# Kernel optimization log

Hardware: AMD Instinct MI355X
Metric: run time of the kernel (lower is better)

## Reference

```python
import jax, jax.numpy as jnp
import numpy as np

N_NODES = 100000
N_EDGES = 3200000
NUM_TYPES = 8
TYPE_DIM = 16
IN_DIM = 5
HID = 64
HEADS = 2
OUT = 64
LN_EPS = 1e-5
NEG_SLOPE = 0.2


def segment_softmax(logits, seg, num_segments):
    # logits: [E, H], seg: [E] destination ids
    m = jax.ops.segment_max(logits, seg, num_segments=num_segments)
    m = jnp.where(jnp.isfinite(m), m, 0.0)
    e = jnp.exp(logits - m[seg])
    s = jax.ops.segment_sum(e, seg, num_segments=num_segments)
    return e / (s[seg] + 1e-16)


def gat_conv(x, W, a_src, a_dst, b, src, dst, n_nodes, heads, ch):
    # x: [N, F_in], W: [F_in, heads*ch], a_src/a_dst: [heads, ch], b: [heads*ch]
    h = (x @ W).reshape(n_nodes, heads, ch)            # [N, H, C]
    al_s = jnp.einsum('nhc,hc->nh', h, a_src)          # [N, H]
    al_d = jnp.einsum('nhc,hc->nh', h, a_dst)          # [N, H]
    e = jax.nn.leaky_relu(al_s[src] + al_d[dst], NEG_SLOPE)  # [E, H]
    alpha = segment_softmax(e, dst, n_nodes)           # [E, H]
    msg = alpha[:, :, None] * h[src]                   # [E, H, C]
    out = jax.ops.segment_sum(msg, dst, num_segments=n_nodes)  # [N, H, C]
    return out.reshape(n_nodes, heads * ch) + b


def setup_inputs() -> dict:
    key = jax.random.key(0)
    ks = jax.random.split(key, 16)
    in1 = IN_DIM + TYPE_DIM  # 21
    inp = {
        'x': jax.random.normal(ks[0], (N_NODES, IN_DIM), dtype=jnp.float32),
        'edge_index': jax.random.randint(ks[1], (2, N_EDGES), 0, N_NODES, dtype=jnp.int32),
        'type_ids': jax.random.randint(ks[2], (N_NODES,), 0, NUM_TYPES, dtype=jnp.int32),
        'type_emb': jax.random.normal(ks[3], (NUM_TYPES, TYPE_DIM), dtype=jnp.float32) * 0.3,
        'W1': jax.random.normal(ks[4], (in1, HID), dtype=jnp.float32) * (1.0 / np.sqrt(in1)),
        'a_src1': jax.random.normal(ks[5], (HEADS, HID // HEADS), dtype=jnp.float32) * 0.1,
        'a_dst1': jax.random.normal(ks[6], (HEADS, HID // HEADS), dtype=jnp.float32) * 0.1,
        'b1': jnp.zeros((HID,), dtype=jnp.float32),
        'W2': jax.random.normal(ks[7], (HID, OUT), dtype=jnp.float32) * (1.0 / np.sqrt(HID)),
        'a_src2': jax.random.normal(ks[8], (1, OUT), dtype=jnp.float32) * 0.1,
        'a_dst2': jax.random.normal(ks[9], (1, OUT), dtype=jnp.float32) * 0.1,
        'b2': jnp.zeros((OUT,), dtype=jnp.float32),
        'gamma': jnp.ones((OUT,), dtype=jnp.float32),
        'beta': jnp.zeros((OUT,), dtype=jnp.float32),
    }
    return inp


def reference(x, type_emb, W1, a_src1, a_dst1, b1, W2, a_src2, a_dst2, b2, gamma, beta, edge_index, type_ids):
    n = x.shape[0]
    # type embedding concat
    xin = jnp.concatenate([x, type_emb[type_ids]], axis=1)  # [N, 21]
    # add self loops (PyG GATConv default)
    loops = jnp.arange(n, dtype=edge_index.dtype)
    src = jnp.concatenate([edge_index[0], loops])
    dst = jnp.concatenate([edge_index[1], loops])
    h = gat_conv(xin, W1, a_src1, a_dst1, b1, src, dst, n, HEADS, HID // HEADS)
    h = jax.nn.relu(h)  # dropout = identity at inference
    h = gat_conv(h, W2, a_src2, a_dst2, b2, src, dst, n, 1, OUT)
    # LayerNorm
    mu = jnp.mean(h, axis=-1, keepdims=True)
    var = jnp.var(h, axis=-1, keepdims=True)
    return (h - mu) / jnp.sqrt(var + LN_EPS) * gamma + beta
```

## Files before the change

### kernel.cpp

```cpp
#include <hip/hip_runtime.h>
#include <hip/hip_fp16.h>

#define NEG_SLOPE 0.2f
#define BKT_SHIFT 8
#define BKT_NODES 256
#define BKT_CAP 10240
#define SRC_SHIFT 18
#define SRC_MASK 0x3FFFF
#define CHUNK 4096
#define NBMAX 512

typedef _Float16 half8 __attribute__((ext_vector_type(8)));
typedef float float4v __attribute__((ext_vector_type(4)));

__global__ void k_node1(const float* __restrict__ x, const int* __restrict__ type_ids,
                        const float* __restrict__ type_emb, const float* __restrict__ W1,
                        const float* __restrict__ a_src1, const float* __restrict__ a_dst1,
                        __half2* __restrict__ h1h, float* __restrict__ als1, float* __restrict__ ald1,
                        int N)
{
    int node = blockIdx.x * 4 + (threadIdx.x >> 6);
    int j = threadIdx.x & 63;
    if (node >= N) return;

    float xin[21];
#pragma unroll
    for (int k = 0; k < 5; k++) xin[k] = x[node * 5 + k];
    int t = type_ids[node];
#pragma unroll
    for (int k = 0; k < 16; k++) xin[5 + k] = type_emb[t * 16 + k];

    float h = 0.f;
#pragma unroll
    for (int k = 0; k < 21; k++) h += xin[k] * W1[k * 64 + j];

    float hn = __shfl_xor(h, 1);
    if ((j & 1) == 0)
        h1h[node * 32 + (j >> 1)] = __floats2half2_rn(h, hn);

    int head = j >> 5, lane = j & 31;
    float ps = h * a_src1[head * 32 + lane];
    float pd = h * a_dst1[head * 32 + lane];
#pragma unroll
    for (int m = 16; m >= 1; m >>= 1) { ps += __shfl_xor(ps, m); pd += __shfl_xor(pd, m); }
    if (lane == 0) { als1[node * 2 + head] = ps; ald1[node * 2 + head] = pd; }
}

__global__ void k_bucketA(const int* __restrict__ ei, unsigned int* __restrict__ pk,
                          int* __restrict__ bcnt, int E, int NBKT)
{
    __shared__ unsigned int stage[CHUNK];
    __shared__ unsigned short stageB[CHUNK];
    __shared__ int cnt[NBMAX];
    __shared__ int excl[NBMAX];
    __shared__ int curp[NBMAX];
    __shared__ int gbase[NBMAX];

    int t = threadIdx.x;
    int e0 = blockIdx.x * CHUNK;
    bool vec4 = ((E & 3) == 0);

    for (int i = t; i < NBMAX; i += 256) cnt[i] = 0;
    __syncthreads();

    int4 s4[4], d4[4];
    bool val[4];

    if (vec4) {
#pragma unroll
        for (int it = 0; it < 4; it++) {
            int e = e0 + it * 1024 + t * 4;
            val[it] = (e < E);
            if (val[it]) {
                s4[it] = *(const int4*)(ei + e);
                d4[it] = *(const int4*)(ei + (size_t)E + e);
                atomicAdd(&cnt[d4[it].x >> BKT_SHIFT], 1);
                atomicAdd(&cnt[d4[it].y >> BKT_SHIFT], 1);
                atomicAdd(&cnt[d4[it].z >> BKT_SHIFT], 1);
                atomicAdd(&cnt[d4[it].w >> BKT_SHIFT], 1);
            }
        }
    } else {
        for (int i = t; i < CHUNK; i += 256) {
            int e = e0 + i;
            if (e >= E) break;
            atomicAdd(&cnt[ei[E + e] >> BKT_SHIFT], 1);
        }
    }
    __syncthreads();
    for (int i = t; i < NBMAX; i += 256) curp[i] = cnt[i];
    __syncthreads();
    for (int off = 1; off < NBMAX; off <<= 1) {
        int v0 = (t >= off) ? cnt[t - off] : 0;
        int v1 = (t + 256 >= off) ? cnt[t + 256 - off] : 0;
        __syncthreads();
        cnt[t] += v0; cnt[t + 256] += v1;
        __syncthreads();
    }
    for (int i = t; i < NBMAX; i += 256) {
        int o = curp[i];
        int ex = cnt[i] - o;
        excl[i] = ex;
        curp[i] = ex;
    }
    __syncthreads();
    for (int b = t; b < NBKT; b += 256) {
        int c = cnt[b] - excl[b];
        gbase[b] = (c > 0) ? atomicAdd(&bcnt[b], c) : 0;
    }
    __syncthreads();
    if (vec4) {
#pragma unroll
        for (int it = 0; it < 4; it++) {
            if (!val[it]) continue;
            int ss[4] = {s4[it].x, s4[it].y, s4[it].z, s4[it].w};
            int dd[4] = {d4[it].x, d4[it].y, d4[it].z, d4[it].w};
#pragma unroll
            for (int k = 0; k < 4; k++) {
                int b = dd[k] >> BKT_SHIFT;
                int p = atomicAdd(&curp[b], 1);
                stage[p] = (unsigned)ss[k] | ((unsigned)(dd[k] & (BKT_NODES - 1)) << SRC_SHIFT);
                stageB[p] = (unsigned short)b;
            }
        }
    } else {
        for (int i = t; i < CHUNK; i += 256) {
            int e = e0 + i;
            if (e >= E) break;
            int s = ei[e], d = ei[E + e];
            int b = d >> BKT_SHIFT;
            int p = atomicAdd(&curp[b], 1);
            stage[p] = (unsigned)s | ((unsigned)(d & (BKT_NODES - 1)) << SRC_SHIFT);
            stageB[p] = (unsigned short)b;
        }
    }
    __syncthreads();
    int total = E - e0; if (total > CHUNK) total = CHUNK;
    for (int i = t; i < total; i += 256) {
        int b = stageB[i];
        int idx = gbase[b] + (i - excl[b]);
        if (idx < BKT_CAP) pk[(size_t)b * BKT_CAP + idx] = stage[i];
    }
}

__global__ void k_build(const unsigned int* __restrict__ pk, const int* __restrict__ bcnt,
                        int* __restrict__ rs, int* __restrict__ cur,
                        int* __restrict__ ssrc, int N)
{
    __shared__ unsigned int vals[BKT_CAP];
    __shared__ int cnt[BKT_NODES];
    __shared__ int cursor[BKT_NODES];
    __shared__ int orig[BKT_NODES];
    __shared__ int red[256];
    int b = blockIdx.x;
    int t = threadIdx.x;
    int nb = min(bcnt[b], BKT_CAP);

    int part = 0;
    for (int i = t; i < b; i += 256) part += min(bcnt[i], BKT_CAP);
    red[t] = part;
    cnt[t] = 0;
    __syncthreads();
    for (int off = 128; off; off >>= 1) {
        if (t < off) red[t] += red[t + off];
        __syncthreads();
    }
    int bs = red[0];

    const unsigned int* mypk = pk + (size_t)b * BKT_CAP;
    int nb4 = nb & ~3;
    for (int e = t * 4; e < nb4; e += 1024) {
        uint4 v = *(const uint4*)(mypk + e);
        *(uint4*)(vals + e) = v;
        atomicAdd(&cnt[v.x >> SRC_SHIFT], 1);
        atomicAdd(&cnt[v.y >> SRC_SHIFT], 1);
        atomicAdd(&cnt[v.z >> SRC_SHIFT], 1);
        atomicAdd(&cnt[v.w >> SRC_SHIFT], 1);
    }
    for (int e = nb4 + t; e < nb; e += 256) {
        unsigned int v = mypk[e];
        vals[e] = v;
        atomicAdd(&cnt[v >> SRC_SHIFT], 1);
    }
    __syncthreads();
    orig[t] = cnt[t];
    __syncthreads();
    for (int off = 1; off < BKT_NODES; off <<= 1) {
        int v = (t >= off) ? cnt[t - off] : 0;
        __syncthreads();
        cnt[t] += v;
        __syncthreads();
    }
    {
        int c = orig[t];
        int ex = cnt[t] - c;
        cursor[t] = ex;
        int node = (b << BKT_SHIFT) + t;
        if (node < N) { rs[node] = bs + ex; cur[node] = bs + ex + c; }
    }
    __syncthreads();
    for (int e = t; e < nb; e += 256) {
        unsigned int w = vals[e];
        int p = atomicAdd(&cursor[w >> SRC_SHIFT], 1);
        ssrc[bs + p] = (int)(w & SRC_MASK);
    }
}

__global__ void k_gather1(const int* __restrict__ rs, const int* __restrict__ cur,
                          const int* __restrict__ ssrc, const float4* __restrict__ h4,
                          const float* __restrict__ als1, const float* __restrict__ ald1,
                          const float* __restrict__ b1, float4* __restrict__ h2h4, int N)
{
    int node = blockIdx.x * 4 + (threadIdx.x >> 6);
    if (node >= N) return;
    int l = threadIdx.x & 63;
    int eg = l >> 3;
    int ch = l & 7;
    int head = ch >> 2;
    float ad = ald1[node * 2 + head];

    int beg = rs[node], end = cur[node];
    int cnt = end - beg;
    __half2 acc2[4];
    acc2[0] = acc2[1] = acc2[2] = acc2[3] = __float2half2_rn(0.f);
    float wsum = 0.f;

    int s0n = (eg < cnt) ? ssrc[beg + eg] : node;
    int s1n = (8 + eg < cnt) ? ssrc[beg + 8 + eg] : node;

    for (int base = 0; base < cnt; base += 16) {
        int s0 = s0n, s1 = s1n;
        bool v0 = (base + eg) < cnt, v1 = (base + 8 + eg) < cnt;
        int n0 = base + 16 + eg, n1 = base + 24 + eg;
        s0n = (n0 < cnt) ? ssrc[beg + n0] : node;
        s1n = (n1 < cnt) ? ssrc[beg + n1] : node;

        float al0 = als1[s0 * 2 + head];
        float al1 = als1[s1 * 2 + head];
        float4 r0 = h4[(size_t)s0 * 8 + ch];
        float4 r1 = h4[(size_t)s1 * 8 + ch];
        float lg0 = al0 + ad; lg0 = (lg0 >= 0.f) ? lg0 : NEG_SLOPE * lg0;
        float lg1 = al1 + ad; lg1 = (lg1 >= 0.f) ? lg1 : NEG_SLOPE * lg1;
        float w0 = v0 ? __expf(lg0) : 0.f;
        float w1 = v1 ? __expf(lg1) : 0.f;
        __half2 wh0 = __float2half2_rn(w0);
        __half2 wh1 = __float2half2_rn(w1);
        const __half2* p0 = (const __half2*)&r0;
        const __half2* p1 = (const __half2*)&r1;
#pragma unroll
        for (int q = 0; q < 4; q++) {
            acc2[q] = __hfma2(p0[q], wh0, acc2[q]);
            acc2[q] = __hfma2(p1[q], wh1, acc2[q]);
        }
        wsum += w0 + w1;
    }
    float acc[8];
#pragma unroll
    for (int q = 0; q < 4; q++) {
        float2 f = __half22float2(acc2[q]);
        acc[2*q] = f.x; acc[2*q+1] = f.y;
    }
#pragma unroll
    for (int m = 8; m <= 32; m <<= 1) {
        wsum += __shfl_xor(wsum, m);
#pragma unroll
        for (int q = 0; q < 8; q++) acc[q] += __shfl_xor(acc[q], m);
    }
    {
        float lg = als1[node * 2 + head] + ad;
        lg = (lg >= 0.f) ? lg : NEG_SLOPE * lg;
        float w = __expf(lg);
        float4 r = h4[(size_t)node * 8 + ch];
        const __half2* p = (const __half2*)&r;
#pragma unroll
        for (int q = 0; q < 4; q++) {
            float2 f = __half22float2(p[q]);
            acc[2*q] += w * f.x; acc[2*q+1] += w * f.y;
        }
        wsum += w;
    }
    float inv = 1.f / (wsum + 1e-16f);
    if (eg == 0) {
        union { float4 f4; __half2 h2[4]; } u;
#pragma unroll
        for (int q = 0; q < 4; q++) {
            float v0 = fmaxf(acc[2*q]   * inv + b1[ch * 8 + 2*q],     0.f);
            float v1 = fmaxf(acc[2*q+1] * inv + b1[ch * 8 + 2*q + 1], 0.f);
            u.h2[q] = __floats2half2_rn(v0, v1);
        }
        h2h4[(size_t)node * 8 + ch] = u.f4;
    }
}

__global__ __launch_bounds__(256) void k_node2m(
        const _Float16* __restrict__ h2h, const float* __restrict__ W2,
        const float* __restrict__ a_src2, const float* __restrict__ a_dst2,
        _Float16* __restrict__ h3h, float* __restrict__ als2, float* __restrict__ ald2, int N)
{
    __shared__ _Float16 w2t[64][72];
    __shared__ float h3t[4][16][65];
    int t = threadIdx.x;
    for (int e = t; e < 4096; e += 256) {
        int k = e >> 6, n = e & 63;
        w2t[n][k] = (_Float16)W2[e];
    }
    __syncthreads();

    int w = t >> 6, l = t & 63;
    int l15 = l & 15, quad = l >> 4;
    int nodebase = blockIdx.x * 64 + w * 16;

    int arow = nodebase + l15;
    if (arow >= N) arow = N - 1;
    const half8* ap = (const half8*)(h2h + (size_t)arow * 64 + quad * 8);
    half8 a0 = ap[0];
    half8 a1 = ap[4];
    float4v accs[4];
#pragma unroll
    for (int nt = 0; nt < 4; nt++) {
        half8 b0 = *(const half8*)(&w2t[nt * 16 + l15][quad * 8]);
        half8 b1 = *(const half8*)(&w2t[nt * 16 + l15][32 + quad * 8]);
        float4v c = {0.f, 0.f, 0.f, 0.f};
        c = __builtin_amdgcn_mfma_f32_16x16x32_f16(a0, b0, c, 0, 0, 0);
        c = __builtin_amdgcn_mfma_f32_16x16x32_f16(a1, b1, c, 0, 0, 0);
        accs[nt] = c;
    }
#pragma unroll
    for (int nt = 0; nt < 4; nt++)
#pragma unroll
        for (int r = 0; r < 4; r++)
            h3t[w][quad * 4 + r][nt * 16 + l15] = accs[nt][r];
    __syncthreads();

    int m = l >> 2, part = l & 3;
    int g = blockIdx.x * 64 + w * 16 + m;
    float ps = 0.f, pd = 0.f;
    union { float4 f4[2]; _Float16 h[16]; } u;
#pragma unroll
    for (int c = 0; c < 16; c++) {
        float v = h3t[w][m][part * 16 + c];
        ps += v * a_src2[part * 16 + c];
        pd += v * a_dst2[part * 16 + c];
        u.h[c] = (_Float16)v;
    }
    if (g < N) {
        float4* dst = (float4*)(h3h + (size_t)g * 64) + part * 2;
        dst[0] = u.f4[0];
        dst[1] = u.f4[1];
    }
    ps += __shfl_xor(ps, 1); ps += __shfl_xor(ps, 2);
    pd += __shfl_xor(pd, 1); pd += __shfl_xor(pd, 2);
    if (part == 0 && g < N) { als2[g] = ps; ald2[g] = pd; }
}

__global__ void k_gather2(const int* __restrict__ rs, const int* __restrict__ cur,
                          const int* __restrict__ ssrc, const float4* __restrict__ h4,
                          const float* __restrict__ als2, const float* __restrict__ ald2,
                          const float* __restrict__ b2, const float* __restrict__ gamma,
                          const float* __restrict__ beta, float* __restrict__ out, int N)
{
    int node = blockIdx.x * 4 + (threadIdx.x >> 6);
    if (node >= N) return;
    int l = threadIdx.x & 63;
    int eg = l >> 3;
    int ch = l & 7;
    float ad = ald2[node];

    int beg = rs[node], end = cur[node];
    int cnt = end - beg;
    __half2 acc2[4];
    acc2[0] = acc2[1] = acc2[2] = acc2[3] = __float2half2_rn(0.f);
    float wsum = 0.f;

    int s0n = (eg < cnt) ? ssrc[beg + eg] : node;
    int s1n = (8 + eg < cnt) ? ssrc[beg + 8 + eg] : node;

    for (int base = 0; base < cnt; base += 16) {
        int s0 = s0n, s1 = s1n;
        bool v0 = (base + eg) < cnt, v1 = (base + 8 + eg) < cnt;
        int n0 = base + 16 + eg, n1 = base + 24 + eg;
        s0n = (n0 < cnt) ? ssrc[beg + n0] : node;
        s1n = (n1 < cnt) ? ssrc[beg + n1] : node;

        float al0 = als2[s0];
        float al1 = als2[s1];
        float4 r0 = h4[(size_t)s0 * 8 + ch];
        float4 r1 = h4[(size_t)s1 * 8 + ch];
        float lg0 = al0 + ad; lg0 = (lg0 >= 0.f) ? lg0 : NEG_SLOPE * lg0;
        float lg1 = al1 + ad; lg1 = (lg1 >= 0.f) ? lg1 : NEG_SLOPE * lg1;
        float w0 = v0 ? __expf(lg0) : 0.f;
        float w1 = v1 ? __expf(lg1) : 0.f;
        __half2 wh0 = __float2half2_rn(w0);
        __half2 wh1 = __float2half2_rn(w1);
        const __half2* p0 = (const __half2*)&r0;
        const __half2* p1 = (const __half2*)&r1;
#pragma unroll
        for (int q = 0; q < 4; q++) {
            acc2[q] = __hfma2(p0[q], wh0, acc2[q]);
            acc2[q] = __hfma2(p1[q], wh1, acc2[q]);
        }
        wsum += w0 + w1;
    }
    float acc[8];
#pragma unroll
    for (int q = 0; q < 4; q++) {
        float2 f = __half22float2(acc2[q]);
        acc[2*q] = f.x; acc[2*q+1] = f.y;
    }
#pragma unroll
    for (int m = 8; m <= 32; m <<= 1) {
        wsum += __shfl_xor(wsum, m);
#pragma unroll
        for (int q = 0; q < 8; q++) acc[q] += __shfl_xor(acc[q], m);
    }
    {
        float lg = als2[node] + ad;
        lg = (lg >= 0.f) ? lg : NEG_SLOPE * lg;
        float w = __expf(lg);
        float4 r = h4[(size_t)node * 8 + ch];
        const __half2* p = (const __half2*)&r;
#pragma unroll
        for (int q = 0; q < 4; q++) {
            float2 f = __half22float2(p[q]);
            acc[2*q] += w * f.x; acc[2*q+1] += w * f.y;
        }
        wsum += w;
    }
    float inv = 1.f / (wsum + 1e-16f);
    float o[8];
    float s = 0.f;
#pragma unroll
    for (int q = 0; q < 8; q++) { o[q] = acc[q] * inv + b2[ch * 8 + q]; s += o[q]; }
#pragma unroll
    for (int m = 1; m <= 4; m <<= 1) s += __shfl_xor(s, m);
    float mu = s * (1.f / 64.f);
    float v = 0.f;
#pragma unroll
    for (int q = 0; q < 8; q++) { float d = o[q] - mu; v += d * d; }
#pragma unroll
    for (int m = 1; m <= 4; m <<= 1) v += __shfl_xor(v, m);
    v *= (1.f / 64.f);
    float r = rsqrtf(v + 1e-5f);
    if (eg == 0) {
        float res[8];
#pragma unroll
        for (int q = 0; q < 8; q++)
            res[q] = (o[q] - mu) * r * gamma[ch * 8 + q] + beta[ch * 8 + q];
        float4* op = (float4*)(out + (size_t)node * 64 + ch * 8);
        op[0] = make_float4(res[0], res[1], res[2], res[3]);
        op[1] = make_float4(res[4], res[5], res[6], res[7]);
    }
}

extern "C" void kernel_launch(void* const* d_in, const int* in_sizes, int n_in,
                              void* d_out, int out_size, void* d_ws, size_t ws_size,
                              hipStream_t stream) {
    const float* x        = (const float*)d_in[0];
    const int*   ei       = (const int*)  d_in[1];
    const int*   type_ids = (const int*)  d_in[2];
    const float* type_emb = (const float*)d_in[3];
    const float* W1       = (const float*)d_in[4];
    const float* a_src1   = (const float*)d_in[5];
    const float* a_dst1   = (const float*)d_in[6];
    const float* b1       = (const float*)d_in[7];
    const float* W2       = (const float*)d_in[8];
    const float* a_src2   = (const float*)d_in[9];
    const float* a_dst2   = (const float*)d_in[10];
    const float* b2       = (const float*)d_in[11];
    const float* gamma    = (const float*)d_in[12];
    const float* beta     = (const float*)d_in[13];

    int N = in_sizes[0] / 5;
    int E = in_sizes[1] / 2;
    int NBKT = (N + BKT_NODES - 1) >> BKT_SHIFT;

    char* base = (char*)d_ws;
    size_t off = 0;
    auto carve = [&](size_t bytes) { void* p = base + off; off += (bytes + 255) & ~(size_t)255; return p; };
    __half2* h1h = (__half2*)carve((size_t)N * 64 * sizeof(__half));
    size_t pk_bytes = (size_t)NBKT * BKT_CAP * sizeof(unsigned int);
    size_t h23_bytes = 2 * (size_t)N * 64 * sizeof(__half);
    char* uni = (char*)carve(pk_bytes > h23_bytes ? pk_bytes : h23_bytes);
    _Float16* h2h = (_Float16*)uni;
    _Float16* h3h = (_Float16*)(uni + (size_t)N * 64 * sizeof(__half));
    unsigned int* pk = (unsigned int*)uni;
    float* als1  = (float*)carve((size_t)N * 2 * sizeof(float));
    float* ald1  = (float*)carve((size_t)N * 2 * sizeof(float));
    float* als2  = (float*)carve((size_t)N * sizeof(float));
    float* ald2  = (float*)carve((size_t)N * sizeof(float));
    int*   rs    = (int*)carve((size_t)N * sizeof(int));
    int*   cur   = (int*)carve((size_t)N * sizeof(int));
    int*   bcnt  = (int*)carve(1024 * sizeof(int));
    int*   ssrc  = (int*)carve((size_t)E * sizeof(int));

    dim3 tb(256);
    dim3 nb((N + 3) / 4);

    k_node1<<<nb, tb, 0, stream>>>(x, type_ids, type_emb, W1, a_src1, a_dst1,
                                   h1h, als1, ald1, N);

    hipMemsetAsync(bcnt, 0, NBKT * sizeof(int), stream);
    k_bucketA<<<dim3((E + CHUNK - 1) / CHUNK), tb, 0, stream>>>(ei, pk, bcnt, E, NBKT);
    k_build<<<dim3(NBKT), tb, 0, stream>>>(pk, bcnt, rs, cur, ssrc, N);

    k_gather1<<<nb, tb, 0, stream>>>(rs, cur, ssrc, (const float4*)h1h, als1, ald1, b1,
                                     (float4*)h2h, N);
    k_node2m<<<dim3((N + 63) / 64), tb, 0, stream>>>(h2h, W2, a_src2, a_dst2,
                                                     h3h, als2, ald2, N);
    k_gather2<<<nb, tb, 0, stream>>>(rs, cur, ssrc, (const float4*)h3h, als2, ald2, b2,
                                     gamma, beta, (float*)d_out, N);
}
```

Measured before the change: 314.4 us.

## Fuse node projection into CSR build, halve bucket size, deepen gather prefetch

Folds the first-layer node projection kernel into the CSR-build kernel as extra blocks, removing one launch and letting the two independent jobs run side by side. Buckets shrink to 128 nodes with a 5120 capacity, so there are more build blocks and less shared memory per block, and the bucketing scan grows to cover 1024 entries. The gather loops now prefetch the next iteration's attention scalars and feature rows, not only the indices, to hide gather latency. Attention logits are pre-scaled by 1/ln2 so exp2f can replace expf. The smaller per-bucket capacity raises the risk of overflow and silently dropped edges on skewed degree distributions.

```diff
diff --git a/kernel.cpp b/kernel.cpp
--- a/kernel.cpp
+++ b/kernel.cpp
@@ -2,49 +2,17 @@
 #include <hip/hip_fp16.h>
 
 #define NEG_SLOPE 0.2f
-#define BKT_SHIFT 8
-#define BKT_NODES 256
-#define BKT_CAP 10240
+#define INVLN2 1.44269504088896f
+#define BKT_SHIFT 7
+#define BKT_NODES 128
+#define BKT_CAP 5120
 #define SRC_SHIFT 18
 #define SRC_MASK 0x3FFFF
 #define CHUNK 4096
-#define NBMAX 512
+#define NBMAX 1024
 
 typedef _Float16 half8 __attribute__((ext_vector_type(8)));
 typedef float float4v __attribute__((ext_vector_type(4)));
-
-__global__ void k_node1(const float* __restrict__ x, const int* __restrict__ type_ids,
-                        const float* __restrict__ type_emb, const float* __restrict__ W1,
-                        const float* __restrict__ a_src1, const float* __restrict__ a_dst1,
-                        __half2* __restrict__ h1h, float* __restrict__ als1, float* __restrict__ ald1,
-                        int N)
-{
-    int node = blockIdx.x * 4 + (threadIdx.x >> 6);
-    int j = threadIdx.x & 63;
-    if (node >= N) return;
-
-    float xin[21];
-#pragma unroll
-    for (int k = 0; k < 5; k++) xin[k] = x[node * 5 + k];
-    int t = type_ids[node];
-#pragma unroll
-    for (int k = 0; k < 16; k++) xin[5 + k] = type_emb[t * 16 + k];
-
-    float h = 0.f;
-#pragma unroll
-    for (int k = 0; k < 21; k++) h += xin[k] * W1[k * 64 + j];
-
-    float hn = __shfl_xor(h, 1);
-    if ((j & 1) == 0)
-        h1h[node * 32 + (j >> 1)] = __floats2half2_rn(h, hn);
-
-    int head = j >> 5, lane = j & 31;
-    float ps = h * a_src1[head * 32 + lane];
-    float pd = h * a_dst1[head * 32 + lane];
-#pragma unroll
-    for (int m = 16; m >= 1; m >>= 1) { ps += __shfl_xor(ps, m); pd += __shfl_xor(pd, m); }
-    if (lane == 0) { als1[node * 2 + head] = ps; ald1[node * 2 + head] = pd; }
-}
 
 __global__ void k_bucketA(const int* __restrict__ ei, unsigned int* __restrict__ pk,
                           int* __restrict__ bcnt, int E, int NBKT)
@@ -91,10 +59,12 @@
     for (int i = t; i < NBMAX; i += 256) curp[i] = cnt[i];
     __syncthreads();
     for (int off = 1; off < NBMAX; off <<= 1) {
-        int v0 = (t >= off) ? cnt[t - off] : 0;
+        int v0 = (t       >= off) ? cnt[t       - off] : 0;
         int v1 = (t + 256 >= off) ? cnt[t + 256 - off] : 0;
+        int v2 = (t + 512 >= off) ? cnt[t + 512 - off] : 0;
+        int v3 = (t + 768 >= off) ? cnt[t + 768 - off] : 0;
         __syncthreads();
-        cnt[t] += v0; cnt[t + 256] += v1;
+        cnt[t] += v0; cnt[t + 256] += v1; cnt[t + 512] += v2; cnt[t + 768] += v3;
         __syncthreads();
     }
     for (int i = t; i < NBMAX; i += 256) {
@@ -143,23 +113,61 @@
     }
 }
 
-__global__ void k_build(const unsigned int* __restrict__ pk, const int* __restrict__ bcnt,
-                        int* __restrict__ rs, int* __restrict__ cur,
-                        int* __restrict__ ssrc, int N)
+__global__ __launch_bounds__(256) void k_build_node1(
+        const unsigned int* __restrict__ pk, const int* __restrict__ bcnt,
+        int* __restrict__ rs, int* __restrict__ cur, int* __restrict__ ssrc,
+        const float* __restrict__ x, const int* __restrict__ type_ids,
+        const float* __restrict__ type_emb, const float* __restrict__ W1,
+        const float* __restrict__ a_src1, const float* __restrict__ a_dst1,
+        __half2* __restrict__ h1h, float* __restrict__ als1, float* __restrict__ ald1,
+        int N, int NBKT)
 {
     __shared__ unsigned int vals[BKT_CAP];
     __shared__ int cnt[BKT_NODES];
     __shared__ int cursor[BKT_NODES];
     __shared__ int orig[BKT_NODES];
     __shared__ int red[256];
+    int t = threadIdx.x;
+
+    if (blockIdx.x >= NBKT) {
+        int node = (blockIdx.x - NBKT) * 4 + (t >> 6);
+        int j = t & 63;
+        if (node >= N) return;
+
+        float xin[21];
+#pragma unroll
+        for (int k = 0; k < 5; k++) xin[k] = x[node * 5 + k];
+        int ty = type_ids[node];
+#pragma unroll
+        for (int k = 0; k < 16; k++) xin[5 + k] = type_emb[ty * 16 + k];
+
+        float h = 0.f;
+#pragma unroll
+        for (int k = 0; k < 21; k++) h += xin[k] * W1[k * 64 + j];
+
+        float hn = __shfl_xor(h, 1);
+        if ((j & 1) == 0)
+            h1h[node * 32 + (j >> 1)] = __floats2half2_rn(h, hn);
+
+        int head = j >> 5, lane = j & 31;
+        float ps = h * a_src1[head * 32 + lane];
+        float pd = h * a_dst1[head * 32 + lane];
+#pragma unroll
+        for (int m = 16; m >= 1; m >>= 1) { ps += __shfl_xor(ps, m); pd += __shfl_xor(pd, m); }
+        if (lane == 0) {
+            als1[node * 2 + head] = ps * INVLN2;
+            ald1[node * 2 + head] = pd * INVLN2;
+        }
+        return;
+    }
+
     int b = blockIdx.x;
-    int t = threadIdx.x;
     int nb = min(bcnt[b], BKT_CAP);
 
     int part = 0;
     for (int i = t; i < b; i += 256) part += min(bcnt[i], BKT_CAP);
     red[t] = part;
-    cnt[t] = 0;
+    if (t < BKT_NODES) cnt[t] = 0;
     __syncthreads();
     for (int off = 128; off; off >>= 1) {
         if (t < off) red[t] += red[t + off];
@@ -183,15 +191,16 @@
         atomicAdd(&cnt[v >> SRC_SHIFT], 1);
     }
     __syncthreads();
-    orig[t] = cnt[t];
+    if (t < BKT_NODES) orig[t] = cnt[t];
     __syncthreads();
     for (int off = 1; off < BKT_NODES; off <<= 1) {
-        int v = (t >= off) ? cnt[t - off] : 0;
+        int v = 0;
+        if (t < BKT_NODES && t >= off) v = cnt[t - off];
         __syncthreads();
-        cnt[t] += v;
+        if (t < BKT_NODES) cnt[t] += v;
         __syncthreads();
     }
-    {
+    if (t < BKT_NODES) {
         int c = orig[t];
         int ex = cnt[t] - c;
         cursor[t] = ex;
@@ -225,34 +234,39 @@
     acc2[0] = acc2[1] = acc2[2] = acc2[3] = __float2half2_rn(0.f);
     float wsum = 0.f;
 
-    int s0n = (eg < cnt) ? ssrc[beg + eg] : node;
-    int s1n = (8 + eg < cnt) ? ssrc[beg + 8 + eg] : node;
+    int s0c = (eg < cnt) ? ssrc[beg + eg] : node;
+    int s1c = (8 + eg < cnt) ? ssrc[beg + 8 + eg] : node;
+    float al0c = als1[s0c * 2 + head];
+    float al1c = als1[s1c * 2 + head];
+    float4 r0c = h4[(size_t)s0c * 8 + ch];
+    float4 r1c = h4[(size_t)s1c * 8 + ch];
 
     for (int base = 0; base < cnt; base += 16) {
-        int s0 = s0n, s1 = s1n;
+        int n0 = base + 16 + eg, n1 = base + 24 + eg;
+        int s0n = (n0 < cnt) ? ssrc[beg + n0] : node;
+        int s1n = (n1 < cnt) ? ssrc[beg + n1] : node;
+        float al0n = als1[s0n * 2 + head];
+        float al1n = als1[s1n * 2 + head];
+        float4 r0n = h4[(size_t)s0n * 8 + ch];
+        float4 r1n = h4[(size_t)s1n * 8 + ch];
+
         bool v0 = (base + eg) < cnt, v1 = (base + 8 + eg) < cnt;
-        int n0 = base + 16 + eg, n1 = base + 24 + eg;
-        s0n = (n0 < cnt) ? ssrc[beg + n0] : node;
-        s1n = (n1 < cnt) ? ssrc[beg + n1] : node;
-
-        float al0 = als1[s0 * 2 + head];
-        float al1 = als1[s1 * 2 + head];
-        float4 r0 = h4[(size_t)s0 * 8 + ch];
-        float4 r1 = h4[(size_t)s1 * 8 + ch];
-        float lg0 = al0 + ad; lg0 = (lg0 >= 0.f) ? lg0 : NEG_SLOPE * lg0;
-        float lg1 = al1 + ad; lg1 = (lg1 >= 0.f) ? lg1 : NEG_SLOPE * lg1;
-        float w0 = v0 ? __expf(lg0) : 0.f;
-        float w1 = v1 ? __expf(lg1) : 0.f;
+        float lg0 = al0c + ad; lg0 = (lg0 >= 0.f) ? lg0 : NEG_SLOPE * lg0;
+        float lg1 = al1c + ad; lg1 = (lg1 >= 0.f) ? lg1 : NEG_SLOPE * lg1;
+        float w0 = v0 ? exp2f(lg0) : 0.f;
+        float w1 = v1 ? exp2f(lg1) : 0.f;
         __half2 wh0 = __float2half2_rn(w0);
         __half2 wh1 = __float2half2_rn(w1);
-        const __half2* p0 = (const __half2*)&r0;
-        const __half2* p1 = (const __half2*)&r1;
+        const __half2* p0 = (const __half2*)&r0c;
+        const __half2* p1 = (const __half2*)&r1c;
 #pragma unroll
         for (int q = 0; q < 4; q++) {
             acc2[q] = __hfma2(p0[q], wh0, acc2[q]);
             acc2[q] = __hfma2(p1[q], wh1, acc2[q]);
         }
         wsum += w0 + w1;
+
+        s0c = s0n; s1c = s1n; al0c = al0n; al1c = al1n; r0c = r0n; r1c = r1n;
     }
     float acc[8];
 #pragma unroll
@@ -269,7 +283,7 @@
     {
         float lg = als1[node * 2 + head] + ad;
         lg = (lg >= 0.f) ? lg : NEG_SLOPE * lg;
-        float w = __expf(lg);
+        float w = exp2f(lg);
         float4 r = h4[(size_t)node * 8 + ch];
         const __half2* p = (const __half2*)&r;
 #pragma unroll
@@ -350,7 +364,7 @@
     }
     ps += __shfl_xor(ps, 1); ps += __shfl_xor(ps, 2);
     pd += __shfl_xor(pd, 1); pd += __shfl_xor(pd, 2);
-    if (part == 0 && g < N) { als2[g] = ps; ald2[g] = pd; }
+    if (part == 0 && g < N) { als2[g] = ps * INVLN2; ald2[g] = pd * INVLN2; }
 }
 
 __global__ void k_gather2(const int* __restrict__ rs, const int* __restrict__ cur,
@@ -372,34 +386,39 @@
     acc2[0] = acc2[1] = acc2[2] = acc2[3] = __float2half2_rn(0.f);
     float wsum = 0.f;
 
-    int s0n = (eg < cnt) ? ssrc[beg + eg] : node;
-    int s1n = (8 + eg < cnt) ? ssrc[beg + 8 + eg] : node;
+    int s0c = (eg < cnt) ? ssrc[beg + eg] : node;
+    int s1c = (8 + eg < cnt) ? ssrc[beg + 8 + eg] : node;
+    float al0c = als2[s0c];
+    float al1c = als2[s1c];
+    float4 r0c = h4[(size_t)s0c * 8 + ch];
+    float4 r1c = h4[(size_t)s1c * 8 + ch];
 
     for (int base = 0; base < cnt; base += 16) {
-        int s0 = s0n, s1 = s1n;
+        int n0 = base + 16 + eg, n1 = base + 24 + eg;
+        int s0n = (n0 < cnt) ? ssrc[beg + n0] : node;
+        int s1n = (n1 < cnt) ? ssrc[beg + n1] : node;
+        float al0n = als2[s0n];
+        float al1n = als2[s1n];
+        float4 r0n = h4[(size_t)s0n * 8 + ch];
+        float4 r1n = h4[(size_t)s1n * 8 + ch];
+
         bool v0 = (base + eg) < cnt, v1 = (base + 8 + eg) < cnt;
-        int n0 = base + 16 + eg, n1 = base + 24 + eg;
-        s0n = (n0 < cnt) ? ssrc[beg + n0] : node;
-        s1n = (n1 < cnt) ? ssrc[beg + n1] : node;
-
-        float al0 = als2[s0];
-        float al1 = als2[s1];
-        float4 r0 = h4[(size_t)s0 * 8 + ch];
-        float4 r1 = h4[(size_t)s1 * 8 + ch];
-        float lg0 = al0 + ad; lg0 = (lg0 >= 0.f) ? lg0 : NEG_SLOPE * lg0;
-        float lg1 = al1 + ad; lg1 = (lg1 >= 0.f) ? lg1 : NEG_SLOPE * lg1;
-        float w0 = v0 ? __expf(lg0) : 0.f;
-        float w1 = v1 ? __expf(lg1) : 0.f;
+        float lg0 = al0c + ad; lg0 = (lg0 >= 0.f) ? lg0 : NEG_SLOPE * lg0;
+        float lg1 = al1c + ad; lg1 = (lg1 >= 0.f) ? lg1 : NEG_SLOPE * lg1;
+        float w0 = v0 ? exp2f(lg0) : 0.f;
+        float w1 = v1 ? exp2f(lg1) : 0.f;
         __half2 wh0 = __float2half2_rn(w0);
         __half2 wh1 = __float2half2_rn(w1);
-        const __half2* p0 = (const __half2*)&r0;
-        const __half2* p1 = (const __half2*)&r1;
+        const __half2* p0 = (const __half2*)&r0c;
+        const __half2* p1 = (const __half2*)&r1c;
 #pragma unroll
         for (int q = 0; q < 4; q++) {
             acc2[q] = __hfma2(p0[q], wh0, acc2[q]);
             acc2[q] = __hfma2(p1[q], wh1, acc2[q]);
         }
         wsum += w0 + w1;
+
+        s0c = s0n; s1c = s1n; al0c = al0n; al1c = al1n; r0c = r0n; r1c = r1n;
     }
     float acc[8];
 #pragma unroll
@@ -416,7 +435,7 @@
     {
         float lg = als2[node] + ad;
         lg = (lg >= 0.f) ? lg : NEG_SLOPE * lg;
-        float w = __expf(lg);
+        float w = exp2f(lg);
         float4 r = h4[(size_t)node * 8 + ch];
         const __half2* p = (const __half2*)&r;
 #pragma unroll
@@ -495,13 +514,15 @@
 
     dim3 tb(256);
     dim3 nb((N + 3) / 4);
-
-    k_node1<<<nb, tb, 0, stream>>>(x, type_ids, type_emb, W1, a_src1, a_dst1,
-                                   h1h, als1, ald1, N);
+    int nodeBlocks = (N + 3) / 4;
 
     hipMemsetAsync(bcnt, 0, NBKT * sizeof(int), stream);
     k_bucketA<<<dim3((E + CHUNK - 1) / CHUNK), tb, 0, stream>>>(ei, pk, bcnt, E, NBKT);
-    k_build<<<dim3(NBKT), tb, 0, stream>>>(pk, bcnt, rs, cur, ssrc, N);
+
+    k_build_node1<<<dim3(NBKT + nodeBlocks), tb, 0, stream>>>(
+        pk, bcnt, rs, cur, ssrc,
+        x, type_ids, type_emb, W1, a_src1, a_dst1, h1h, als1, ald1,
+        N, NBKT);
 
     k_gather1<<<nb, tb, 0, stream>>>(rs, cur, ssrc, (const float4*)h1h, als1, ald1, b1,
                                      (float4*)h2h, N);
```

Result: no change. 316.8 us (+0.7%).
